# Kernel tuning notes

Hardware: AMD Instinct MI355X
Metric: run time of the kernel (lower is better)

The kernel has to match this reference:

```python
import jax, jax.numpy as jnp
import numpy as np

ALPHA = 1.5
N_ITER = 50


def _p(z):
    # p(z) = max(z, 0) ** (1/(alpha-1)); for alpha=1.5 this is relu(z)**2
    return jnp.maximum(z, 0.0) ** (1.0 / (ALPHA - 1.0))


def _entmax_core(X):
    # Bisection search for the entmax threshold tau (entmax_bisect, dim=-1).
    d = X.shape[-1]
    Xs = X * (ALPHA - 1.0)
    max_val = jnp.max(Xs, axis=-1, keepdims=True)
    tau_lo = max_val - 1.0                                  # gp_inv(1, alpha) = 1
    tau_hi = max_val - (1.0 / d) ** (ALPHA - 1.0)           # gp_inv(1/d, alpha)
    f_lo = jnp.sum(_p(Xs - tau_lo), axis=-1, keepdims=True) - 1.0
    dm = tau_hi - tau_lo

    def body(carry, _):
        tau_lo, dm, _ = carry
        dm = dm * 0.5
        tau_m = tau_lo + dm
        f_m = jnp.sum(_p(Xs - tau_m), axis=-1, keepdims=True) - 1.0
        tau_lo = jnp.where(f_m * f_lo >= 0, tau_m, tau_lo)
        return (tau_lo, dm, tau_m), None

    (_, _, tau_m), _ = jax.lax.scan(body, (tau_lo, dm, tau_lo), None, length=N_ITER)
    p = _p(Xs - tau_m)                                      # last midpoint, as in torch code
    return p / jnp.sum(p, axis=-1, keepdims=True)           # ensure_sum_one=True


@jax.custom_vjp
def entmax_bisect(X):
    return _entmax_core(X)


def _entmax_fwd(X):
    p = _entmax_core(X)
    return p, p


def _entmax_bwd(p, dY):
    # Exact implicit gradient used by entmax's custom autograd backward.
    gppr = jnp.where(p > 0, p ** (2.0 - ALPHA), 0.0)
    dX = dY * gppr
    q = jnp.sum(dX, axis=-1, keepdims=True) / jnp.sum(gppr, axis=-1, keepdims=True)
    return (dX - q * gppr,)


entmax_bisect.defvjp(_entmax_fwd, _entmax_bwd)


def setup_inputs() -> dict:
    key = jax.random.key(0)
    # small spread keeps the entmax support dense so log(p) is finite everywhere
    X = 0.002 * jax.random.normal(key, (4096, 32000), dtype=jnp.float32)
    return {"X": X}


def reference(X):
    p = entmax_bisect(X)
    p = p / jnp.sum(p, axis=1, keepdims=True)  # redundant renorm, as in the module
    return jnp.log(p)
```

## Files before the change

kernel.cpp:

```cpp
#include <hip/hip_runtime.h>
#include <math.h>


constexpr int D     = 32000;
constexpr int BLOCK = 640;
constexpr int NW    = BLOCK / 64;
constexpr int VPT   = D / BLOCK;
constexpr int V2    = VPT / 2;

__global__ __launch_bounds__(BLOCK) void
log_entmax_kernel(const float* __restrict__ X, float* __restrict__ out) {
    const int row  = blockIdx.x;
    const int tid  = threadIdx.x;
    const int lane = tid & 63;
    const int wave = tid >> 6;

    __shared__ float red[NW][4];

    const float2* __restrict__ src = reinterpret_cast<const float2*>(X + (size_t)row * D);
    float2* __restrict__       dst = reinterpret_cast<float2*>(out + (size_t)row * D);

    float xs[VPT];
#pragma unroll
    for (int j = 0; j < V2; ++j) {
        float2 v = src[j * BLOCK + tid];
        xs[2 * j]     = 0.5f * v.x;
        xs[2 * j + 1] = 0.5f * v.y;
    }

    float tau = -INFINITY;
    for (int it = 0; it < 16; ++it) {
        float k = 0.f, s1 = 0.f, q = 0.f;
#pragma unroll
        for (int j = 0; j < VPT; ++j) {
            float v = xs[j];
            if (v > tau) { k += 1.f; s1 += v; q += v * v; }
        }
#pragma unroll
        for (int o = 32; o > 0; o >>= 1) {
            k  += __shfl_down(k, o);
            s1 += __shfl_down(s1, o);
            q  += __shfl_down(q, o);
        }
        if (lane == 0) { red[wave][0] = k; red[wave][1] = s1; red[wave][2] = q; }
        __syncthreads();
        k = 0.f; s1 = 0.f; q = 0.f;
#pragma unroll
        for (int w = 0; w < NW; ++w) {
            k += red[w][0]; s1 += red[w][1]; q += red[w][2];
        }
        __syncthreads();

        float mu   = s1 / k;
        float disc = mu * mu - (q - 1.0f) / k;
        float tnew = mu - sqrtf(fmaxf(disc, 0.0f));
        if (tnew == tau) break;
        tau = tnew;
    }

    float S = 0.f;
#pragma unroll
    for (int j = 0; j < VPT; ++j) {
        float z = fmaxf(xs[j] - tau, 0.f);
        S += z * z;
    }
#pragma unroll
    for (int o = 32; o > 0; o >>= 1) S += __shfl_down(S, o);
    if (lane == 0) red[wave][0] = S;
    __syncthreads();
    S = 0.f;
#pragma unroll
    for (int w = 0; w < NW; ++w) S += red[w][0];

    const float lS = __logf(S);

#pragma unroll
    for (int j = 0; j < V2; ++j) {
        float z0 = fmaxf(xs[2 * j]     - tau, 0.f);
        float z1 = fmaxf(xs[2 * j + 1] - tau, 0.f);
        float2 o;
        o.x = 2.f * __logf(z0) - lS;
        o.y = 2.f * __logf(z1) - lS;
        dst[j * BLOCK + tid] = o;
    }
}

extern "C" void kernel_launch(void* const* d_in, const int* in_sizes, int n_in,
                              void* d_out, int out_size, void* d_ws, size_t ws_size,
                              hipStream_t stream) {
    const float* X = (const float*)d_in[0];
    float* out     = (float*)d_out;
    const int rows = in_sizes[0] / D;
    log_entmax_kernel<<<rows, BLOCK, 0, stream>>>(X, out);
}
```

Before: 875.6 us.

## Process several rows per block, prefetching the next row during output writes

```diff
diff --git a/kernel.cpp b/kernel.cpp
--- a/kernel.cpp
+++ b/kernel.cpp
@@ -7,81 +7,108 @@
 constexpr int NW    = BLOCK / 64;
 constexpr int VPT   = D / BLOCK;
 constexpr int V2    = VPT / 2;
+constexpr int RPB   = 8;
 
 __global__ __launch_bounds__(BLOCK) void
-log_entmax_kernel(const float* __restrict__ X, float* __restrict__ out) {
-    const int row  = blockIdx.x;
+log_entmax_kernel(const float* __restrict__ X, float* __restrict__ out, int nrows) {
     const int tid  = threadIdx.x;
     const int lane = tid & 63;
     const int wave = tid >> 6;
 
     __shared__ float red[NW][4];
 
-    const float2* __restrict__ src = reinterpret_cast<const float2*>(X + (size_t)row * D);
-    float2* __restrict__       dst = reinterpret_cast<float2*>(out + (size_t)row * D);
+    const int row0 = blockIdx.x * RPB;
 
     float xs[VPT];
+    {
+        const float2* __restrict__ src =
+            reinterpret_cast<const float2*>(X + (size_t)row0 * D);
 #pragma unroll
-    for (int j = 0; j < V2; ++j) {
-        float2 v = src[j * BLOCK + tid];
-        xs[2 * j]     = 0.5f * v.x;
-        xs[2 * j + 1] = 0.5f * v.y;
+        for (int j = 0; j < V2; ++j) {
+            float2 v = src[j * BLOCK + tid];
+            xs[2 * j]     = 0.5f * v.x;
+            xs[2 * j + 1] = 0.5f * v.y;
+        }
     }
 
-    float tau = -INFINITY;
-    for (int it = 0; it < 16; ++it) {
-        float k = 0.f, s1 = 0.f, q = 0.f;
+    for (int r = 0; r < RPB; ++r) {
+        const int row = row0 + r;
+
+        float tau = -INFINITY;
+        for (int it = 0; it < 16; ++it) {
+            float k = 0.f, s1 = 0.f, q = 0.f;
+#pragma unroll
+            for (int j = 0; j < VPT; ++j) {
+                float v = xs[j];
+                if (v > tau) { k += 1.f; s1 += v; q += v * v; }
+            }
+#pragma unroll
+            for (int o = 32; o > 0; o >>= 1) {
+                k  += __shfl_down(k, o);
+                s1 += __shfl_down(s1, o);
+                q  += __shfl_down(q, o);
+            }
+            if (lane == 0) { red[wave][0] = k; red[wave][1] = s1; red[wave][2] = q; }
+            __syncthreads();
+            k = 0.f; s1 = 0.f; q = 0.f;
+#pragma unroll
+            for (int w = 0; w < NW; ++w) {
+                k += red[w][0]; s1 += red[w][1]; q += red[w][2];
+            }
+            __syncthreads();
+
+            float mu   = s1 / k;
+            float disc = mu * mu - (q - 1.0f) / k;
+            float tnew = mu - sqrtf(fmaxf(disc, 0.0f));
+            if (tnew == tau) break;
+            tau = tnew;
+        }
+
+        float S = 0.f;
 #pragma unroll
         for (int j = 0; j < VPT; ++j) {
-            float v = xs[j];
-            if (v > tau) { k += 1.f; s1 += v; q += v * v; }
+            float z = fmaxf(xs[j] - tau, 0.f);
+            S += z * z;
         }
 #pragma unroll
-        for (int o = 32; o > 0; o >>= 1) {
-            k  += __shfl_down(k, o);
-            s1 += __shfl_down(s1, o);
-            q  += __shfl_down(q, o);
-        }
-        if (lane == 0) { red[wave][0] = k; red[wave][1] = s1; red[wave][2] = q; }
+        for (int o = 32; o > 0; o >>= 1) S += __shfl_down(S, o);
+        if (lane == 0) red[wave][0] = S;
         __syncthreads();
-        k = 0.f; s1 = 0.f; q = 0.f;
+        S = 0.f;
 #pragma unroll
-        for (int w = 0; w < NW; ++w) {
-            k += red[w][0]; s1 += red[w][1]; q += red[w][2];
-        }
+        for (int w = 0; w < NW; ++w) S += red[w][0];
         __syncthreads();
 
-        float mu   = s1 / k;
-        float disc = mu * mu - (q - 1.0f) / k;
-        float tnew = mu - sqrtf(fmaxf(disc, 0.0f));
-        if (tnew == tau) break;
-        tau = tnew;
-    }
+        const float lS = __logf(S);
 
-    float S = 0.f;
+        float2* __restrict__ dst = reinterpret_cast<float2*>(out + (size_t)row * D);
+
+        if (r + 1 < RPB) {
+            const float2* __restrict__ nsrc =
+                reinterpret_cast<const float2*>(X + (size_t)(row + 1) * D);
 #pragma unroll
-    for (int j = 0; j < VPT; ++j) {
-        float z = fmaxf(xs[j] - tau, 0.f);
-        S += z * z;
-    }
+            for (int j = 0; j < V2; ++j) {
+                float2 nv = nsrc[j * BLOCK + tid];
+                float z0 = fmaxf(xs[2 * j]     - tau, 0.f);
+                float z1 = fmaxf(xs[2 * j + 1] - tau, 0.f);
+                float2 o;
+                o.x = 2.f * __logf(z0) - lS;
+                o.y = 2.f * __logf(z1) - lS;
+                dst[j * BLOCK + tid] = o;
+                xs[2 * j]     = 0.5f * nv.x;
+                xs[2 * j + 1] = 0.5f * nv.y;
+            }
+        } else {
 #pragma unroll
-    for (int o = 32; o > 0; o >>= 1) S += __shfl_down(S, o);
-    if (lane == 0) red[wave][0] = S;
-    __syncthreads();
-    S = 0.f;
-#pragma unroll
-    for (int w = 0; w < NW; ++w) S += red[w][0];
-
-    const float lS = __logf(S);
-
-#pragma unroll
-    for (int j = 0; j < V2; ++j) {
-        float z0 = fmaxf(xs[2 * j]     - tau, 0.f);
-        float z1 = fmaxf(xs[2 * j + 1] - tau, 0.f);
-        float2 o;
-        o.x = 2.f * __logf(z0) - lS;
-        o.y = 2.f * __logf(z1) - lS;
-        dst[j * BLOCK + tid] = o;
+            for (int j = 0; j < V2; ++j) {
+                float z0 = fmaxf(xs[2 * j]     - tau, 0.f);
+                float z1 = fmaxf(xs[2 * j + 1] - tau, 0.f);
+                float2 o;
+                o.x = 2.f * __logf(z0) - lS;
+                o.y = 2.f * __logf(z1) - lS;
+                dst[j * BLOCK + tid] = o;
+            }
+        }
     }
 }
 
@@ -91,5 +118,5 @@
     const float* X = (const float*)d_in[0];
     float* out     = (float*)d_out;
     const int rows = in_sizes[0] / D;
-    log_entmax_kernel<<<rows, BLOCK, 0, stream>>>(X, out);
+    log_entmax_kernel<<<rows / RPB, BLOCK, 0, stream>>>(X, out, rows);
 }
```

New measurement: 916.1 us. 1.05x slower.

## Seed threshold from full-support moments and derive final sum algebraically

Applied to the files above, without the earlier changes.

```diff
diff --git a/kernel.cpp b/kernel.cpp
--- a/kernel.cpp
+++ b/kernel.cpp
@@ -8,7 +8,7 @@
 constexpr int VPT   = D / BLOCK;
 constexpr int V2    = VPT / 2;
 
-__global__ __launch_bounds__(BLOCK) void
+__global__ __launch_bounds__(BLOCK, 5) void
 log_entmax_kernel(const float* __restrict__ X, float* __restrict__ out) {
     const int row  = blockIdx.x;
     const int tid  = threadIdx.x;
@@ -21,57 +21,69 @@
     float2* __restrict__       dst = reinterpret_cast<float2*>(out + (size_t)row * D);
 
     float xs[VPT];
+    float s1 = 0.f, q = 0.f;
 #pragma unroll
     for (int j = 0; j < V2; ++j) {
         float2 v = src[j * BLOCK + tid];
-        xs[2 * j]     = 0.5f * v.x;
-        xs[2 * j + 1] = 0.5f * v.y;
+        float a = 0.5f * v.x;
+        float b = 0.5f * v.y;
+        xs[2 * j]     = a;
+        xs[2 * j + 1] = b;
+        s1 += a + b;
+        q  += a * a + b * b;
+    }
+#pragma unroll
+    for (int o = 32; o > 0; o >>= 1) {
+        s1 += __shfl_down(s1, o);
+        q  += __shfl_down(q, o);
+    }
+    if (lane == 0) { red[wave][1] = s1; red[wave][2] = q; }
+    __syncthreads();
+    s1 = 0.f; q = 0.f;
+#pragma unroll
+    for (int w = 0; w < NW; ++w) { s1 += red[w][1]; q += red[w][2]; }
+    __syncthreads();
+
+    float k = (float)D;
+    float tau;
+    {
+        float mu   = s1 / k;
+        float disc = mu * mu - (q - 1.0f) / k;
+        tau = mu - sqrtf(fmaxf(disc, 0.0f));
     }
 
-    float tau = -INFINITY;
     for (int it = 0; it < 16; ++it) {
-        float k = 0.f, s1 = 0.f, q = 0.f;
+        float kk = 0.f, ss = 0.f, qq = 0.f;
 #pragma unroll
         for (int j = 0; j < VPT; ++j) {
             float v = xs[j];
-            if (v > tau) { k += 1.f; s1 += v; q += v * v; }
+            if (v > tau) { kk += 1.f; ss += v; qq += v * v; }
         }
 #pragma unroll
         for (int o = 32; o > 0; o >>= 1) {
-            k  += __shfl_down(k, o);
-            s1 += __shfl_down(s1, o);
-            q  += __shfl_down(q, o);
+            kk += __shfl_down(kk, o);
+            ss += __shfl_down(ss, o);
+            qq += __shfl_down(qq, o);
         }
-        if (lane == 0) { red[wave][0] = k; red[wave][1] = s1; red[wave][2] = q; }
+        if (lane == 0) { red[wave][0] = kk; red[wave][1] = ss; red[wave][2] = qq; }
         __syncthreads();
-        k = 0.f; s1 = 0.f; q = 0.f;
+        kk = 0.f; ss = 0.f; qq = 0.f;
 #pragma unroll
         for (int w = 0; w < NW; ++w) {
-            k += red[w][0]; s1 += red[w][1]; q += red[w][2];
+            kk += red[w][0]; ss += red[w][1]; qq += red[w][2];
         }
-        __syncthreads();
 
-        float mu   = s1 / k;
-        float disc = mu * mu - (q - 1.0f) / k;
+        float mu   = ss / kk;
+        float disc = mu * mu - (qq - 1.0f) / kk;
         float tnew = mu - sqrtf(fmaxf(disc, 0.0f));
+
+        k = kk; s1 = ss; q = qq;
         if (tnew == tau) break;
         tau = tnew;
+        __syncthreads();
     }
 
-    float S = 0.f;
-#pragma unroll
-    for (int j = 0; j < VPT; ++j) {
-        float z = fmaxf(xs[j] - tau, 0.f);
-        S += z * z;
-    }
-#pragma unroll
-    for (int o = 32; o > 0; o >>= 1) S += __shfl_down(S, o);
-    if (lane == 0) red[wave][0] = S;
-    __syncthreads();
-    S = 0.f;
-#pragma unroll
-    for (int w = 0; w < NW; ++w) S += red[w][0];
-
+    const float S  = q - 2.f * tau * s1 + k * tau * tau;
     const float lS = __logf(S);
 
 #pragma unroll
```

Result: slower. 1.440 ms (+64.5%).
